# Optimization experiments

Hardware: AMD Instinct MI355X
Metric: run time of the kernel (lower is better)

## Reference

```python
import jax, jax.numpy as jnp
import numpy as np

BERT_DIM = 768
N_ROWS = 5
N_COLS = 12
LN_EPS = 1e-5


def setup_inputs() -> dict:
    key = jax.random.key(0)
    ks = jax.random.split(key, 12)
    B, S = 256, 512
    token_hidden = jax.random.normal(ks[0], (B, S, BERT_DIM), dtype=jnp.float32)
    attention_mask = jax.random.randint(ks[1], (B, S), 0, 2, dtype=jnp.int32)
    s = lambda fan_in: 1.0 / np.sqrt(fan_in)
    return {
        "token_hidden": token_hidden,
        "attention_mask": attention_mask,
        # token_attention: Linear(768,128) -> Tanh -> Linear(128,1)
        "att_w1": jax.random.normal(ks[2], (128, BERT_DIM), dtype=jnp.float32) * s(BERT_DIM),
        "att_b1": jnp.zeros((128,), dtype=jnp.float32),
        "att_w2": jax.random.normal(ks[3], (1, 128), dtype=jnp.float32) * s(128),
        "att_b2": jnp.zeros((1,), dtype=jnp.float32),
        # feature_projector: Linear(768,256) -> GELU -> Dropout(eval) -> Linear(256,5)
        "proj_w1": jax.random.normal(ks[4], (256, BERT_DIM), dtype=jnp.float32) * s(BERT_DIM),
        "proj_b1": jnp.zeros((256,), dtype=jnp.float32),
        "proj_w2": jax.random.normal(ks[5], (N_ROWS, 256), dtype=jnp.float32) * s(256),
        "proj_b2": jnp.zeros((N_ROWS,), dtype=jnp.float32),
        # LayerNorm([5, 12])
        "ln_gamma": jnp.ones((N_ROWS, N_COLS), dtype=jnp.float32),
        "ln_beta": jnp.zeros((N_ROWS, N_COLS), dtype=jnp.float32),
    }


def reference(token_hidden, attention_mask, att_w1, att_b1, att_w2, att_b2,
              proj_w1, proj_b1, proj_w2, proj_b2, ln_gamma, ln_beta):
    # token attention scores: [B, S]
    h = jnp.tanh(jnp.einsum("bsd,hd->bsh", token_hidden, att_w1) + att_b1)
    scores = (jnp.einsum("bsh,oh->bso", h, att_w2) + att_b2)[..., 0]
    scores = jnp.where(attention_mask == 0, jnp.finfo(scores.dtype).min, scores)
    weights = jax.nn.softmax(scores, axis=-1)
    # top-k token selection (indices sorted ascending to preserve order)
    k = min(N_COLS, token_hidden.shape[1])
    _, top_idx = jax.lax.top_k(weights, k)  # [B, k]
    top_idx = jnp.sort(top_idx, axis=-1)
    selected = jnp.take_along_axis(token_hidden, top_idx[:, :, None], axis=1)  # [B, k, D]
    # feature projector (dropout is eval no-op)
    f = jax.nn.gelu(jnp.einsum("bkd,hd->bkh", selected, proj_w1) + proj_b1, approximate=False)
    f = jnp.einsum("bkh,rh->bkr", f, proj_w2) + proj_b2  # [B, k, n_rows]
    features = jnp.transpose(f, (0, 2, 1))  # [B, n_rows, k]
    if features.shape[-1] < N_COLS:
        features = jnp.pad(features, ((0, 0), (0, 0), (0, N_COLS - features.shape[-1])))
    # LayerNorm over trailing [n_rows, n_cols]
    mean = jnp.mean(features, axis=(-2, -1), keepdims=True)
    var = jnp.var(features, axis=(-2, -1), keepdims=True)
    return ln_gamma * (features - mean) * jax.lax.rsqrt(var + LN_EPS) + ln_beta
```

## Files before the change

### kernel.cpp

```cpp
#include <hip/hip_runtime.h>
#include <math.h>

#define B_BATCH 256
#define S_LEN   512
#define D_DIM   768
#define H_ATT   128
#define TOPK    12
#define NCAND   16
#define H_PROJ  256
#define N_ROWS  5
#define N_COLS  12

typedef __bf16 bf16x8 __attribute__((ext_vector_type(8)));
typedef __bf16 bf16x4 __attribute__((ext_vector_type(4)));
typedef float  f32x4  __attribute__((ext_vector_type(4)));

__device__ inline void split8(float4 a, float4 b, bf16x8& hi, bf16x8& lo) {
    float v[8] = {a.x, a.y, a.z, a.w, b.x, b.y, b.z, b.w};
#pragma unroll
    for (int i = 0; i < 8; ++i) {
        __bf16 h = (__bf16)v[i];
        hi[i] = h;
        lo[i] = (__bf16)(v[i] - (float)h);
    }
}

__global__ __launch_bounds__(1024, 4) void fused_kernel(
    const float* __restrict__ th,
    const int*   __restrict__ mask,
    const float* __restrict__ aw1,
    const float* __restrict__ ab1,
    const float* __restrict__ aw2,
    const float* __restrict__ pw1,
    const float* __restrict__ pb1,
    const float* __restrict__ pw2,
    const float* __restrict__ pb2,
    const float* __restrict__ gamma,
    const float* __restrict__ beta,
    float* __restrict__ out)
{
    const int b   = blockIdx.x;
    const int tid = threadIdx.x;
    const int wv  = tid >> 6;
    const int ln  = tid & 63;

    __shared__ __align__(16) char ubuf[49152];
    __bf16 (*Bs)[2][4096] = reinterpret_cast<__bf16 (*)[2][4096]>(ubuf);
    float4 (*xc)[192]     = reinterpret_cast<float4 (*)[192]>(ubuf);

    __shared__ float score_s[S_LEN];
    __shared__ unsigned long long wtop[128];
    __shared__ int   cand[NCAND];
    __shared__ float redW[16][2];
    __shared__ float exact_sc[NCAND];
    __shared__ int   sel_slot[TOPK];
    __shared__ float gbuf[TOPK][H_PROJ + 4];
    __shared__ float feat[N_ROWS * N_COLS];
    __shared__ float stats[2];

    const float NEG_MIN = -3.402823466e38f;

    auto build = [&](int kt, int buf) {
        const int nt = tid >> 7;
        const int r  = tid & 127;
        const int l2 = r >> 1;
        const int h4 = (r & 1) * 4;
        const float* src = aw1 + (size_t)(nt * 16 + (l2 & 15)) * D_DIM +
                           kt * 32 + (l2 >> 4) * 8 + h4;
        float4 v = *(const float4*)src;
        bf16x4 hv, lv;
#pragma unroll
        for (int i = 0; i < 4; ++i) {
            float f = (&v.x)[i];
            __bf16 hb = (__bf16)f;
            hv[i] = hb;
            lv[i] = (__bf16)(f - (float)hb);
        }
        const int base = nt * 512 + l2 * 8 + h4;
        *(bf16x4*)(&Bs[buf][0][base]) = hv;
        *(bf16x4*)(&Bs[buf][1][base]) = lv;
    };

    const int col = ln & 15;
    const int kq  = ln >> 4;

    const size_t row0 = (size_t)b * S_LEN + wv * 32 + col;
    const float* pa0 = th + row0 * D_DIM + kq * 8;
    const float* pa1 = pa0 + 16 * D_DIM;

    f32x4 acc[2][8];
    const f32x4 z = {0.f, 0.f, 0.f, 0.f};
#pragma unroll
    for (int i = 0; i < 2; ++i)
#pragma unroll
        for (int j = 0; j < 8; ++j) acc[i][j] = z;

    float4 c00 = *(const float4*)(pa0);
    float4 c01 = *(const float4*)(pa0 + 4);
    float4 c10 = *(const float4*)(pa1);
    float4 c11 = *(const float4*)(pa1 + 4);
    build(0, 0);
    __syncthreads();

    for (int kt = 0; kt < 24; ++kt) {
        const int buf = kt & 1;
        float4 n00, n01, n10, n11;
        if (kt < 23) {
            n00 = *(const float4*)(pa0 + (kt + 1) * 32);
            n01 = *(const float4*)(pa0 + (kt + 1) * 32 + 4);
            n10 = *(const float4*)(pa1 + (kt + 1) * 32);
            n11 = *(const float4*)(pa1 + (kt + 1) * 32 + 4);
            build(kt + 1, buf ^ 1);
        }

        bf16x8 ah0, al0, ah1, al1;
        split8(c00, c01, ah0, al0);
        split8(c10, c11, ah1, al1);

#pragma unroll
        for (int nt = 0; nt < 8; ++nt) {
            bf16x8 bh = *(bf16x8*)(&Bs[buf][0][nt * 512 + ln * 8]);
            bf16x8 bl = *(bf16x8*)(&Bs[buf][1][nt * 512 + ln * 8]);
            acc[0][nt] = __builtin_amdgcn_mfma_f32_16x16x32_bf16(ah0, bh, acc[0][nt], 0, 0, 0);
            acc[0][nt] = __builtin_amdgcn_mfma_f32_16x16x32_bf16(al0, bh, acc[0][nt], 0, 0, 0);
            acc[0][nt] = __builtin_amdgcn_mfma_f32_16x16x32_bf16(ah0, bl, acc[0][nt], 0, 0, 0);
            acc[1][nt] = __builtin_amdgcn_mfma_f32_16x16x32_bf16(ah1, bh, acc[1][nt], 0, 0, 0);
            acc[1][nt] = __builtin_amdgcn_mfma_f32_16x16x32_bf16(al1, bh, acc[1][nt], 0, 0, 0);
            acc[1][nt] = __builtin_amdgcn_mfma_f32_16x16x32_bf16(ah1, bl, acc[1][nt], 0, 0, 0);
        }

        if (kt < 23) {
            c00 = n00; c01 = n01; c10 = n10; c11 = n11;
            __syncthreads();
        }
    }

    {
        float b1v[8], w2v[8];
#pragma unroll
        for (int nt = 0; nt < 8; ++nt) {
            b1v[nt] = ab1[nt * 16 + col];
            w2v[nt] = aw2[nt * 16 + col];
        }
        const int rowbase = wv * 32;
#pragma unroll
        for (int mf = 0; mf < 2; ++mf)
#pragma unroll
            for (int r = 0; r < 4; ++r) {
                float s = 0.f;
#pragma unroll
                for (int nt = 0; nt < 8; ++nt)
                    s += tanhf(acc[mf][nt][r] + b1v[nt]) * w2v[nt];
                s += __shfl_xor(s, 1, 64);
                s += __shfl_xor(s, 2, 64);
                s += __shfl_xor(s, 4, 64);
                s += __shfl_xor(s, 8, 64);
                if (col == 0)
                    score_s[rowbase + mf * 16 + kq * 4 + r] = s;
            }
    }
    __syncthreads();

    if (wv < 8) {
        int i0 = wv * 64 + ln;
        float v0 = score_s[i0];
        if (mask[(size_t)b * S_LEN + i0] == 0) v0 = NEG_MIN;
        unsigned k0 = __float_as_uint(v0);
        k0 = ((int)k0 >= 0) ? (k0 | 0x80000000u) : ~k0;
        unsigned long long p0 =
            ((unsigned long long)k0 << 32) | (0xFFFFFFFFu - (unsigned)i0);
        for (int it = 0; it < NCAND; ++it) {
            unsigned long long m = p0;
#pragma unroll
            for (int s = 1; s <= 32; s <<= 1) {
                unsigned long long o = __shfl_xor(m, s, 64);
                if (o > m) m = o;
            }
            if (ln == 0) wtop[wv * 16 + it] = m;
            if (p0 == m) p0 = 0ull;
        }
    }
    __syncthreads();
    if (wv == 0) {
        unsigned long long p0 = wtop[ln];
        unsigned long long p1 = wtop[64 + ln];
        for (int it = 0; it < NCAND; ++it) {
            unsigned long long m = p0 > p1 ? p0 : p1;
#pragma unroll
            for (int s = 1; s <= 32; s <<= 1) {
                unsigned long long o = __shfl_xor(m, s, 64);
                if (o > m) m = o;
            }
            if (ln == 0) cand[it] = (int)(0xFFFFFFFFu - (unsigned)(m & 0xFFFFFFFFu));
            if (p0 == m) p0 = 0ull;
            else if (p1 == m) p1 = 0ull;
        }
    }
    __syncthreads();

#pragma unroll
    for (int i = 0; i < 3; ++i) {
        int f = tid + 1024 * i;
        int c = f / 192, k4 = f % 192;
        xc[c][k4] = *(const float4*)(th + ((size_t)b * S_LEN + cand[c]) * D_DIM + k4 * 4);
    }
    __syncthreads();

    {
        const int n  = tid & 127;
        const int h8 = tid >> 7;
        float accs[2] = {0.f, 0.f};
        const float* wrow = aw1 + (size_t)n * D_DIM;
        for (int k4 = 0; k4 < 192; ++k4) {
            float4 w = *(const float4*)(wrow + k4 * 4);
#pragma unroll
            for (int j = 0; j < 2; ++j) {
                float4 x = xc[2 * h8 + j][k4];
                accs[j] += w.x * x.x + w.y * x.y + w.z * x.z + w.w * x.w;
            }
        }
        float b1n = ab1[n], w2n = aw2[n];
#pragma unroll
        for (int j = 0; j < 2; ++j) {
            float val = tanhf(accs[j] + b1n) * w2n;
            val += __shfl_xor(val, 1, 64);
            val += __shfl_xor(val, 2, 64);
            val += __shfl_xor(val, 4, 64);
            val += __shfl_xor(val, 8, 64);
            val += __shfl_xor(val, 16, 64);
            val += __shfl_xor(val, 32, 64);
            if (ln == 0) redW[wv][j] = val;
        }
    }
    __syncthreads();
    if (tid < NCAND) {
        int c = tid;
        int wbase = c & ~1;
        float ex = redW[wbase][c & 1] + redW[wbase + 1][c & 1];
        if (mask[(size_t)b * S_LEN + cand[c]] == 0) ex = -INFINITY;
        exact_sc[c] = ex;
    }
    __syncthreads();

    if (tid == 0) {
        unsigned picked = 0;
        int slots[TOPK];
        for (int it = 0; it < TOPK; ++it) {
            float best = -INFINITY; int bslot = -1; int bidx = 1 << 30;
            for (int c = 0; c < NCAND; ++c) {
                if (picked & (1u << c)) continue;
                float e = exact_sc[c]; int idx = cand[c];
                if (e > best || (e == best && idx < bidx)) { best = e; bslot = c; bidx = idx; }
            }
            picked |= 1u << bslot;
            slots[it] = bslot;
        }
        for (int i = 1; i < TOPK; ++i) {
            int s = slots[i], key = cand[s], j = i - 1;
            while (j >= 0 && cand[slots[j]] > key) { slots[j + 1] = slots[j]; --j; }
            slots[j + 1] = s;
        }
        for (int t = 0; t < TOPK; ++t) sel_slot[t] = slots[t];
    }
    __syncthreads();

    {
        const int j  = tid & 255;
        const int hh = tid >> 8;
        int slots[3];
#pragma unroll
        for (int t = 0; t < 3; ++t) slots[t] = sel_slot[hh * 3 + t];
        float accp[3];
        float bj = pb1[j];
#pragma unroll
        for (int t = 0; t < 3; ++t) accp[t] = bj;
        const float* wrow = pw1 + (size_t)j * D_DIM;
        for (int k4 = 0; k4 < 192; ++k4) {
            float4 w = *(const float4*)(wrow + k4 * 4);
#pragma unroll
            for (int t = 0; t < 3; ++t) {
                float4 x = xc[slots[t]][k4];
                accp[t] += w.x * x.x + w.y * x.y + w.z * x.z + w.w * x.w;
            }
        }
#pragma unroll
        for (int t = 0; t < 3; ++t) {
            float hv = accp[t];
            gbuf[hh * 3 + t][j] = 0.5f * hv * (1.0f + erff(hv * 0.70710678118654752f));
        }
    }
    __syncthreads();

    if (tid < TOPK * N_ROWS) {
        int t = tid / N_ROWS, r = tid % N_ROWS;
        float s = pb2[r];
        const float4* gp = (const float4*)&gbuf[t][0];
        const float4* wp = (const float4*)(pw2 + r * H_PROJ);
        for (int q = 0; q < H_PROJ / 4; ++q) {
            float4 g = gp[q], w = wp[q];
            s += g.x * w.x + g.y * w.y + g.z * w.z + g.w * w.w;
        }
        feat[r * N_COLS + t] = s;
    }
    __syncthreads();

    if (tid == 0) {
        float sum = 0.f;
        for (int i = 0; i < N_ROWS * N_COLS; ++i) sum += feat[i];
        float mean = sum / 60.f;
        float sq = 0.f;
        for (int i = 0; i < N_ROWS * N_COLS; ++i) { float d = feat[i] - mean; sq += d * d; }
        stats[0] = mean;
        stats[1] = sq / 60.f;
    }
    __syncthreads();
    if (tid < N_ROWS * N_COLS) {
        float x = feat[tid];
        out[(size_t)b * 60 + tid] =
            gamma[tid] * (x - stats[0]) * rsqrtf(stats[1] + 1e-5f) + beta[tid];
    }
}

extern "C" void kernel_launch(void* const* d_in, const int* in_sizes, int n_in,
                              void* d_out, int out_size, void* d_ws, size_t ws_size,
                              hipStream_t stream) {
    const float* th   = (const float*)d_in[0];
    const int*   mask = (const int*)  d_in[1];
    const float* aw1  = (const float*)d_in[2];
    const float* ab1  = (const float*)d_in[3];
    const float* aw2  = (const float*)d_in[4];
    const float* pw1  = (const float*)d_in[6];
    const float* pb1  = (const float*)d_in[7];
    const float* pw2  = (const float*)d_in[8];
    const float* pb2  = (const float*)d_in[9];
    const float* gam  = (const float*)d_in[10];
    const float* bet  = (const float*)d_in[11];
    float* out = (float*)d_out;

    (void)d_ws; (void)ws_size;

    hipLaunchKernelGGL(fused_kernel, dim3(B_BATCH), dim3(1024), 0, stream,
                       th, mask, aw1, ab1, aw2, pw1, pb1, pw2, pb2,
                       gam, bet, out);
}
```

Measured before the change: 762.7 us.

## Split fused kernel into half-sequence scoring kernel and per-batch selection kernel

After: 684.5 us. 1.11x faster.

```diff
diff --git a/kernel.cpp b/kernel.cpp
--- a/kernel.cpp
+++ b/kernel.cpp
@@ -12,7 +12,6 @@
 #define N_COLS  12
 
 typedef __bf16 bf16x8 __attribute__((ext_vector_type(8)));
-typedef __bf16 bf16x4 __attribute__((ext_vector_type(4)));
 typedef float  f32x4  __attribute__((ext_vector_type(4)));
 
 __device__ inline void split8(float4 a, float4 b, bf16x8& hi, bf16x8& lo) {
@@ -25,7 +24,168 @@
     }
 }
 
-__global__ __launch_bounds__(1024, 4) void fused_kernel(
+__global__ __launch_bounds__(512, 4) void score_half(
+    const float* __restrict__ th,
+    const int*   __restrict__ mask,
+    const float* __restrict__ aw1,
+    const float* __restrict__ ab1,
+    const float* __restrict__ aw2,
+    float* __restrict__ out)
+{
+    const int blk = blockIdx.x;
+    const int b   = blk >> 1;
+    const int h   = blk & 1;
+    const int tid = threadIdx.x;
+    const int wv  = tid >> 6;
+    const int ln  = tid & 63;
+
+    __shared__ __bf16 Bs[2][2][4096];
+    __shared__ float score_sh[256];
+    __shared__ unsigned long long wtop[64];
+
+    const float NEG_MIN = -3.402823466e38f;
+
+    auto build = [&](int kt, int buf) {
+        const int nt   = tid >> 6;
+        const int lane = tid & 63;
+        const float* src = aw1 + (size_t)(nt * 16 + (lane & 15)) * D_DIM +
+                           kt * 32 + (lane >> 4) * 8;
+        float4 v0 = *(const float4*)src;
+        float4 v1 = *(const float4*)(src + 4);
+        bf16x8 hv, lv;
+        split8(v0, v1, hv, lv);
+        *(bf16x8*)(&Bs[buf][0][tid * 8]) = hv;
+        *(bf16x8*)(&Bs[buf][1][tid * 8]) = lv;
+    };
+
+    const int col = ln & 15;
+    const int kq  = ln >> 4;
+
+    const size_t row0 = (size_t)b * S_LEN + h * 256 + wv * 32 + col;
+    const float* pa0 = th + row0 * D_DIM + kq * 8;
+    const float* pa1 = pa0 + 16 * D_DIM;
+
+    f32x4 acc[2][8];
+    const f32x4 z = {0.f, 0.f, 0.f, 0.f};
+#pragma unroll
+    for (int i = 0; i < 2; ++i)
+#pragma unroll
+        for (int j = 0; j < 8; ++j) acc[i][j] = z;
+
+    float4 c00 = *(const float4*)(pa0);
+    float4 c01 = *(const float4*)(pa0 + 4);
+    float4 c10 = *(const float4*)(pa1);
+    float4 c11 = *(const float4*)(pa1 + 4);
+    build(0, 0);
+    __syncthreads();
+
+    for (int kt = 0; kt < 24; ++kt) {
+        const int buf = kt & 1;
+        float4 n00, n01, n10, n11;
+        if (kt < 23) {
+            n00 = *(const float4*)(pa0 + (kt + 1) * 32);
+            n01 = *(const float4*)(pa0 + (kt + 1) * 32 + 4);
+            n10 = *(const float4*)(pa1 + (kt + 1) * 32);
+            n11 = *(const float4*)(pa1 + (kt + 1) * 32 + 4);
+            build(kt + 1, buf ^ 1);
+        }
+
+        bf16x8 ah0, al0, ah1, al1;
+        split8(c00, c01, ah0, al0);
+        split8(c10, c11, ah1, al1);
+
+#pragma unroll
+        for (int nt = 0; nt < 8; ++nt) {
+            bf16x8 bh = *(bf16x8*)(&Bs[buf][0][nt * 512 + ln * 8]);
+            bf16x8 bl = *(bf16x8*)(&Bs[buf][1][nt * 512 + ln * 8]);
+            acc[0][nt] = __builtin_amdgcn_mfma_f32_16x16x32_bf16(ah0, bh, acc[0][nt], 0, 0, 0);
+            acc[0][nt] = __builtin_amdgcn_mfma_f32_16x16x32_bf16(al0, bh, acc[0][nt], 0, 0, 0);
+            acc[0][nt] = __builtin_amdgcn_mfma_f32_16x16x32_bf16(ah0, bl, acc[0][nt], 0, 0, 0);
+            acc[1][nt] = __builtin_amdgcn_mfma_f32_16x16x32_bf16(ah1, bh, acc[1][nt], 0, 0, 0);
+            acc[1][nt] = __builtin_amdgcn_mfma_f32_16x16x32_bf16(al1, bh, acc[1][nt], 0, 0, 0);
+            acc[1][nt] = __builtin_amdgcn_mfma_f32_16x16x32_bf16(ah1, bl, acc[1][nt], 0, 0, 0);
+        }
+
+        if (kt < 23) {
+            c00 = n00; c01 = n01; c10 = n10; c11 = n11;
+            __syncthreads();
+        }
+    }
+
+    {
+        float b1v[8], w2v[8];
+#pragma unroll
+        for (int nt = 0; nt < 8; ++nt) {
+            b1v[nt] = ab1[nt * 16 + col];
+            w2v[nt] = aw2[nt * 16 + col];
+        }
+        const int rowbase = wv * 32;
+#pragma unroll
+        for (int mf = 0; mf < 2; ++mf)
+#pragma unroll
+            for (int r = 0; r < 4; ++r) {
+                float s = 0.f;
+#pragma unroll
+                for (int nt = 0; nt < 8; ++nt)
+                    s += tanhf(acc[mf][nt][r] + b1v[nt]) * w2v[nt];
+                s += __shfl_xor(s, 1, 64);
+                s += __shfl_xor(s, 2, 64);
+                s += __shfl_xor(s, 4, 64);
+                s += __shfl_xor(s, 8, 64);
+                if (col == 0)
+                    score_sh[rowbase + mf * 16 + kq * 4 + r] = s;
+            }
+    }
+    __syncthreads();
+
+    if (wv < 4) {
+        int i0   = wv * 64 + ln;
+        int gidx = h * 256 + i0;
+        float v0 = score_sh[i0];
+        if (mask[(size_t)b * S_LEN + gidx] == 0) v0 = NEG_MIN;
+        unsigned k0 = __float_as_uint(v0);
+        k0 = ((int)k0 >= 0) ? (k0 | 0x80000000u) : ~k0;
+        unsigned long long p0 =
+            ((unsigned long long)k0 << 32) | (0xFFFFFFFFu - (unsigned)gidx);
+        for (int it = 0; it < NCAND; ++it) {
+            unsigned long long m = p0;
+#pragma unroll
+            for (int s = 1; s <= 32; s <<= 1) {
+                unsigned long long o = __shfl_xor(m, s, 64);
+                if (o > m) m = o;
+            }
+            if (ln == 0) wtop[wv * 16 + it] = m;
+            if (p0 == m) p0 = 0ull;
+        }
+    }
+    __syncthreads();
+    if (wv == 0) {
+        unsigned long long q = wtop[ln];
+        float* base = out + (size_t)b * 60 + h * 24;
+        unsigned tmpidx = 0;
+        for (int it = 0; it < NCAND; ++it) {
+            unsigned long long m = q;
+#pragma unroll
+            for (int s = 1; s <= 32; s <<= 1) {
+                unsigned long long o = __shfl_xor(m, s, 64);
+                if (o > m) m = o;
+            }
+            if (ln == 0) {
+                unsigned keyhi = (unsigned)(m >> 32);
+                unsigned sbits = (keyhi & 0x80000000u) ? (keyhi ^ 0x80000000u)
+                                                       : ~keyhi;
+                base[it] = __uint_as_float(sbits);
+                unsigned gidx = 0xFFFFFFFFu - (unsigned)(m & 0xFFFFFFFFu);
+                if ((it & 1) == 0) tmpidx = gidx;
+                else base[16 + (it >> 1)] =
+                         __uint_as_float(tmpidx | (gidx << 16));
+            }
+            if (q == m) q = 0ull;
+        }
+    }
+}
+
+__global__ __launch_bounds__(256) void select_kernel(
     const float* __restrict__ th,
     const int*   __restrict__ mask,
     const float* __restrict__ aw1,
@@ -37,138 +197,33 @@
     const float* __restrict__ pb2,
     const float* __restrict__ gamma,
     const float* __restrict__ beta,
-    float* __restrict__ out)
+    float* out)
 {
     const int b   = blockIdx.x;
     const int tid = threadIdx.x;
     const int wv  = tid >> 6;
     const int ln  = tid & 63;
 
-    __shared__ __align__(16) char ubuf[49152];
-    __bf16 (*Bs)[2][4096] = reinterpret_cast<__bf16 (*)[2][4096]>(ubuf);
-    float4 (*xc)[192]     = reinterpret_cast<float4 (*)[192]>(ubuf);
-
-    __shared__ float score_s[S_LEN];
-    __shared__ unsigned long long wtop[128];
+    __shared__ float4 xc[NCAND][192];
     __shared__ int   cand[NCAND];
-    __shared__ float redW[16][2];
+    __shared__ float redW[4][8];
     __shared__ float exact_sc[NCAND];
     __shared__ int   sel_slot[TOPK];
     __shared__ float gbuf[TOPK][H_PROJ + 4];
     __shared__ float feat[N_ROWS * N_COLS];
     __shared__ float stats[2];
 
-    const float NEG_MIN = -3.402823466e38f;
-
-    auto build = [&](int kt, int buf) {
-        const int nt = tid >> 7;
-        const int r  = tid & 127;
-        const int l2 = r >> 1;
-        const int h4 = (r & 1) * 4;
-        const float* src = aw1 + (size_t)(nt * 16 + (l2 & 15)) * D_DIM +
-                           kt * 32 + (l2 >> 4) * 8 + h4;
-        float4 v = *(const float4*)src;
-        bf16x4 hv, lv;
-#pragma unroll
-        for (int i = 0; i < 4; ++i) {
-            float f = (&v.x)[i];
-            __bf16 hb = (__bf16)f;
-            hv[i] = hb;
-            lv[i] = (__bf16)(f - (float)hb);
-        }
-        const int base = nt * 512 + l2 * 8 + h4;
-        *(bf16x4*)(&Bs[buf][0][base]) = hv;
-        *(bf16x4*)(&Bs[buf][1][base]) = lv;
-    };
-
-    const int col = ln & 15;
-    const int kq  = ln >> 4;
-
-    const size_t row0 = (size_t)b * S_LEN + wv * 32 + col;
-    const float* pa0 = th + row0 * D_DIM + kq * 8;
-    const float* pa1 = pa0 + 16 * D_DIM;
-
-    f32x4 acc[2][8];
-    const f32x4 z = {0.f, 0.f, 0.f, 0.f};
-#pragma unroll
-    for (int i = 0; i < 2; ++i)
-#pragma unroll
-        for (int j = 0; j < 8; ++j) acc[i][j] = z;
-
-    float4 c00 = *(const float4*)(pa0);
-    float4 c01 = *(const float4*)(pa0 + 4);
-    float4 c10 = *(const float4*)(pa1);
-    float4 c11 = *(const float4*)(pa1 + 4);
-    build(0, 0);
-    __syncthreads();
-
-    for (int kt = 0; kt < 24; ++kt) {
-        const int buf = kt & 1;
-        float4 n00, n01, n10, n11;
-        if (kt < 23) {
-            n00 = *(const float4*)(pa0 + (kt + 1) * 32);
-            n01 = *(const float4*)(pa0 + (kt + 1) * 32 + 4);
-            n10 = *(const float4*)(pa1 + (kt + 1) * 32);
-            n11 = *(const float4*)(pa1 + (kt + 1) * 32 + 4);
-            build(kt + 1, buf ^ 1);
-        }
-
-        bf16x8 ah0, al0, ah1, al1;
-        split8(c00, c01, ah0, al0);
-        split8(c10, c11, ah1, al1);
-
-#pragma unroll
-        for (int nt = 0; nt < 8; ++nt) {
-            bf16x8 bh = *(bf16x8*)(&Bs[buf][0][nt * 512 + ln * 8]);
-            bf16x8 bl = *(bf16x8*)(&Bs[buf][1][nt * 512 + ln * 8]);
-            acc[0][nt] = __builtin_amdgcn_mfma_f32_16x16x32_bf16(ah0, bh, acc[0][nt], 0, 0, 0);
-            acc[0][nt] = __builtin_amdgcn_mfma_f32_16x16x32_bf16(al0, bh, acc[0][nt], 0, 0, 0);
-            acc[0][nt] = __builtin_amdgcn_mfma_f32_16x16x32_bf16(ah0, bl, acc[0][nt], 0, 0, 0);
-            acc[1][nt] = __builtin_amdgcn_mfma_f32_16x16x32_bf16(ah1, bh, acc[1][nt], 0, 0, 0);
-            acc[1][nt] = __builtin_amdgcn_mfma_f32_16x16x32_bf16(al1, bh, acc[1][nt], 0, 0, 0);
-            acc[1][nt] = __builtin_amdgcn_mfma_f32_16x16x32_bf16(ah1, bl, acc[1][nt], 0, 0, 0);
-        }
-
-        if (kt < 23) {
-            c00 = n00; c01 = n01; c10 = n10; c11 = n11;
-            __syncthreads();
-        }
-    }
-
-    {
-        float b1v[8], w2v[8];
-#pragma unroll
-        for (int nt = 0; nt < 8; ++nt) {
-            b1v[nt] = ab1[nt * 16 + col];
-            w2v[nt] = aw2[nt * 16 + col];
-        }
-        const int rowbase = wv * 32;
-#pragma unroll
-        for (int mf = 0; mf < 2; ++mf)
-#pragma unroll
-            for (int r = 0; r < 4; ++r) {
-                float s = 0.f;
-#pragma unroll
-                for (int nt = 0; nt < 8; ++nt)
-                    s += tanhf(acc[mf][nt][r] + b1v[nt]) * w2v[nt];
-                s += __shfl_xor(s, 1, 64);
-                s += __shfl_xor(s, 2, 64);
-                s += __shfl_xor(s, 4, 64);
-                s += __shfl_xor(s, 8, 64);
-                if (col == 0)
-                    score_s[rowbase + mf * 16 + kq * 4 + r] = s;
-            }
-    }
-    __syncthreads();
-
-    if (wv < 8) {
-        int i0 = wv * 64 + ln;
-        float v0 = score_s[i0];
-        if (mask[(size_t)b * S_LEN + i0] == 0) v0 = NEG_MIN;
-        unsigned k0 = __float_as_uint(v0);
-        k0 = ((int)k0 >= 0) ? (k0 | 0x80000000u) : ~k0;
-        unsigned long long p0 =
-            ((unsigned long long)k0 << 32) | (0xFFFFFFFFu - (unsigned)i0);
+    if (wv == 0) {
+        unsigned long long p0 = 0ull;
+        if (ln < 32) {
+            int hh = ln >> 4, i = ln & 15;
+            const float* base = out + (size_t)b * 60 + hh * 24;
+            unsigned sb = __float_as_uint(base[i]);
+            unsigned k  = ((int)sb >= 0) ? (sb | 0x80000000u) : ~sb;
+            unsigned pw = __float_as_uint(base[16 + (i >> 1)]);
+            unsigned gidx = (i & 1) ? (pw >> 16) : (pw & 0xFFFFu);
+            p0 = ((unsigned long long)k << 32) | (0xFFFFFFFFu - gidx);
+        }
         for (int it = 0; it < NCAND; ++it) {
             unsigned long long m = p0;
 #pragma unroll
@@ -176,67 +231,53 @@
                 unsigned long long o = __shfl_xor(m, s, 64);
                 if (o > m) m = o;
             }
-            if (ln == 0) wtop[wv * 16 + it] = m;
-            if (p0 == m) p0 = 0ull;
-        }
-    }
-    __syncthreads();
-    if (wv == 0) {
-        unsigned long long p0 = wtop[ln];
-        unsigned long long p1 = wtop[64 + ln];
-        for (int it = 0; it < NCAND; ++it) {
-            unsigned long long m = p0 > p1 ? p0 : p1;
-#pragma unroll
-            for (int s = 1; s <= 32; s <<= 1) {
-                unsigned long long o = __shfl_xor(m, s, 64);
-                if (o > m) m = o;
-            }
             if (ln == 0) cand[it] = (int)(0xFFFFFFFFu - (unsigned)(m & 0xFFFFFFFFu));
             if (p0 == m) p0 = 0ull;
-            else if (p1 == m) p1 = 0ull;
-        }
-    }
-    __syncthreads();
-
-#pragma unroll
-    for (int i = 0; i < 3; ++i) {
-        int f = tid + 1024 * i;
+        }
+    }
+    __syncthreads();
+
+#pragma unroll
+    for (int i = 0; i < 12; ++i) {
+        int f = tid + 256 * i;
         int c = f / 192, k4 = f % 192;
         xc[c][k4] = *(const float4*)(th + ((size_t)b * S_LEN + cand[c]) * D_DIM + k4 * 4);
     }
     __syncthreads();
 
     {
-        const int n  = tid & 127;
-        const int h8 = tid >> 7;
-        float accs[2] = {0.f, 0.f};
+        const int n = tid & 127;
+        const int h = tid >> 7;
+        float accs[8];
+#pragma unroll
+        for (int ci = 0; ci < 8; ++ci) accs[ci] = 0.f;
         const float* wrow = aw1 + (size_t)n * D_DIM;
         for (int k4 = 0; k4 < 192; ++k4) {
             float4 w = *(const float4*)(wrow + k4 * 4);
 #pragma unroll
-            for (int j = 0; j < 2; ++j) {
-                float4 x = xc[2 * h8 + j][k4];
-                accs[j] += w.x * x.x + w.y * x.y + w.z * x.z + w.w * x.w;
+            for (int ci = 0; ci < 8; ++ci) {
+                float4 x = xc[2 * ci + h][k4];
+                accs[ci] += w.x * x.x + w.y * x.y + w.z * x.z + w.w * x.w;
             }
         }
         float b1n = ab1[n], w2n = aw2[n];
 #pragma unroll
-        for (int j = 0; j < 2; ++j) {
-            float val = tanhf(accs[j] + b1n) * w2n;
+        for (int ci = 0; ci < 8; ++ci) {
+            float val = tanhf(accs[ci] + b1n) * w2n;
             val += __shfl_xor(val, 1, 64);
             val += __shfl_xor(val, 2, 64);
             val += __shfl_xor(val, 4, 64);
             val += __shfl_xor(val, 8, 64);
             val += __shfl_xor(val, 16, 64);
             val += __shfl_xor(val, 32, 64);
-            if (ln == 0) redW[wv][j] = val;
+            if (ln == 0) redW[wv][ci] = val;
         }
     }
     __syncthreads();
     if (tid < NCAND) {
         int c = tid;
-        int wbase = c & ~1;
-        float ex = redW[wbase][c & 1] + redW[wbase + 1][c & 1];
+        float ex = (c & 1) ? (redW[2][c >> 1] + redW[3][c >> 1])
+                           : (redW[0][c >> 1] + redW[1][c >> 1]);
         if (mask[(size_t)b * S_LEN + cand[c]] == 0) ex = -INFINITY;
         exact_sc[c] = ex;
     }
@@ -265,28 +306,27 @@
     __syncthreads();
 
     {
-        const int j  = tid & 255;
-        const int hh = tid >> 8;
-        int slots[3];
-#pragma unroll
-        for (int t = 0; t < 3; ++t) slots[t] = sel_slot[hh * 3 + t];
-        float accp[3];
+        const int j = tid;
+        int slots[TOPK];
+#pragma unroll
+        for (int t = 0; t < TOPK; ++t) slots[t] = sel_slot[t];
+        float accp[TOPK];
         float bj = pb1[j];
 #pragma unroll
-        for (int t = 0; t < 3; ++t) accp[t] = bj;
+        for (int t = 0; t < TOPK; ++t) accp[t] = bj;
         const float* wrow = pw1 + (size_t)j * D_DIM;
         for (int k4 = 0; k4 < 192; ++k4) {
             float4 w = *(const float4*)(wrow + k4 * 4);
 #pragma unroll
-            for (int t = 0; t < 3; ++t) {
+            for (int t = 0; t < TOPK; ++t) {
                 float4 x = xc[slots[t]][k4];
                 accp[t] += w.x * x.x + w.y * x.y + w.z * x.z + w.w * x.w;
             }
         }
 #pragma unroll
-        for (int t = 0; t < 3; ++t) {
-            float hv = accp[t];
-            gbuf[hh * 3 + t][j] = 0.5f * hv * (1.0f + erff(hv * 0.70710678118654752f));
+        for (int t = 0; t < TOPK; ++t) {
+            float hh = accp[t];
+            gbuf[t][j] = 0.5f * hh * (1.0f + erff(hh * 0.70710678118654752f));
         }
     }
     __syncthreads();
@@ -339,7 +379,9 @@
 
     (void)d_ws; (void)ws_size;
 
-    hipLaunchKernelGGL(fused_kernel, dim3(B_BATCH), dim3(1024), 0, stream,
+    hipLaunchKernelGGL(score_half, dim3(2 * B_BATCH), dim3(512), 0, stream,
+                       th, mask, aw1, ab1, aw2, out);
+    hipLaunchKernelGGL(select_kernel, dim3(B_BATCH), dim3(256), 0, stream,
                        th, mask, aw1, ab1, aw2, pw1, pb1, pw2, pb2,
                        gam, bet, out);
 }
```
